# Optimization experiments

Measured on AMD Instinct MI355X. Metric: run time of the kernel, lower is better.

## Reference

```python
import jax, jax.numpy as jnp
import numpy as np

N = 50000      # nodes
E = 600000     # edges
P = 200000     # prediction edges
IN = 128       # in_channels
HID = 128      # hidden per head
H1, H2 = 4, 2  # heads
BN_EPS = 1e-5
NEG_SLOPE = 0.2


def _rn(k, shape, scale=0.05):
    return jax.random.normal(k, shape, jnp.float32) * scale


def setup_inputs() -> dict:
    key = jax.random.key(0)
    ks = jax.random.split(key, 24)
    inp = {}
    inp['x'] = jax.random.normal(ks[0], (N, IN), jnp.float32)
    inp['ei'] = jax.random.randint(ks[1], (2, E), 0, N, dtype=jnp.int32)
    inp['pred_edges'] = jax.random.randint(ks[2], (2, P), 0, N, dtype=jnp.int32)
    inp['pert'] = jax.random.normal(ks[3], (N,), jnp.float32)
    inp['pr'] = jax.random.uniform(ks[4], (N,), jnp.float32)
    # GATv2 layer 1: in=IN -> H1 heads x HID
    inp['Wl1'] = _rn(ks[5], (IN, H1 * HID))
    inp['bl1'] = jnp.zeros((H1 * HID,), jnp.float32)
    inp['Wr1'] = _rn(ks[6], (IN, H1 * HID))
    inp['br1'] = jnp.zeros((H1 * HID,), jnp.float32)
    inp['att1'] = _rn(ks[7], (H1, HID))
    inp['bias1'] = jnp.zeros((H1 * HID,), jnp.float32)
    # BatchNorm1d(H1*HID) eval-mode params
    inp['bn1_g'] = jnp.ones((H1 * HID,), jnp.float32)
    inp['bn1_b'] = jnp.zeros((H1 * HID,), jnp.float32)
    inp['bn1_m'] = _rn(ks[8], (H1 * HID,))
    inp['bn1_v'] = jax.random.uniform(ks[9], (H1 * HID,), jnp.float32, 0.5, 1.5)
    # GATv2 layer 2: in=H1*HID -> H2 heads x HID
    inp['Wl2'] = _rn(ks[10], (H1 * HID, H2 * HID))
    inp['bl2'] = jnp.zeros((H2 * HID,), jnp.float32)
    inp['Wr2'] = _rn(ks[11], (H1 * HID, H2 * HID))
    inp['br2'] = jnp.zeros((H2 * HID,), jnp.float32)
    inp['att2'] = _rn(ks[12], (H2, HID))
    inp['bias2'] = jnp.zeros((H2 * HID,), jnp.float32)
    inp['bn2_g'] = jnp.ones((H2 * HID,), jnp.float32)
    inp['bn2_b'] = jnp.zeros((H2 * HID,), jnp.float32)
    inp['bn2_m'] = _rn(ks[13], (H2 * HID,))
    inp['bn2_v'] = jax.random.uniform(ks[14], (H2 * HID,), jnp.float32, 0.5, 1.5)
    # proj: Linear(H2*HID*2 + 2 + 1, 2)
    inp['Wp'] = _rn(ks[15], (H2 * HID * 2 + 3, 2))
    inp['bp'] = jnp.zeros((2,), jnp.float32)
    return inp


def gatv2(x, src, dst, Wl, bl, Wr, br, att, bias, n):
    """GATv2Conv (concat=True): e_ij = att . LeakyReLU(xl_j + xr_i), segment softmax over dst."""
    H, C = att.shape
    xl = (x @ Wl + bl).reshape(n, H, C)
    xr = (x @ Wr + br).reshape(n, H, C)
    e = jax.nn.leaky_relu(xl[src] + xr[dst], NEG_SLOPE)     # [E, H, C]
    score = jnp.einsum('ehc,hc->eh', e, att)                 # [E, H]
    m = jax.ops.segment_max(score, dst, num_segments=n)     # [N, H]
    ex = jnp.exp(score - m[dst])
    denom = jax.ops.segment_sum(ex, dst, num_segments=n)
    alpha = ex / denom[dst]                                  # [E, H]
    out = jax.ops.segment_sum(alpha[:, :, None] * xl[src], dst, num_segments=n)
    return out.reshape(n, H * C) + bias


def batchnorm_eval(h, g, b, m, v):
    return (h - m) * jax.lax.rsqrt(v + BN_EPS) * g + b


def reference(x, ei, pred_edges, pert, pr,
              Wl1, bl1, Wr1, br1, att1, bias1, bn1_g, bn1_b, bn1_m, bn1_v,
              Wl2, bl2, Wr2, br2, att2, bias2, bn2_g, bn2_b, bn2_m, bn2_v,
              Wp, bp):
    n = x.shape[0]
    loop = jnp.arange(n, dtype=ei.dtype)                    # add_self_loops=True
    src = jnp.concatenate([ei[0], loop])
    dst = jnp.concatenate([ei[1], loop])
    h = gatv2(x, src, dst, Wl1, bl1, Wr1, br1, att1, bias1, n)
    h = jax.nn.relu(batchnorm_eval(h, bn1_g, bn1_b, bn1_m, bn1_v))
    h = gatv2(h, src, dst, Wl2, bl2, Wr2, br2, att2, bias2, n)
    z = jax.nn.relu(batchnorm_eval(h, bn2_g, bn2_b, bn2_m, bn2_v))
    s, d = pred_edges[0], pred_edges[1]
    feat = jnp.concatenate([z[s], z[d], pr[s][:, None], pr[d][:, None],
                            (pert[s] * pert[d])[:, None]], axis=1)
    return feat @ Wp + bp
```

## Files before the change

### kernel.cpp

```cpp
#include <hip/hip_runtime.h>
#include <math.h>

#define BN_EPS 1e-5f
#define N_NODES 50000
#define M_PAD   50048
#define E_EDGES 600000

typedef __attribute__((ext_vector_type(8))) short bf16x8;
typedef __attribute__((ext_vector_type(4))) short bf16x4;
typedef __attribute__((ext_vector_type(4))) float f32x4;

__device__ __forceinline__ short f2bf(float f) {
    unsigned u = __float_as_uint(f);
    u += 0x7fffu + ((u >> 16) & 1u);
    return (short)(u >> 16);
}
__device__ __forceinline__ float bf2f(short s) {
    return __uint_as_float(((unsigned)(unsigned short)s) << 16);
}
__device__ __forceinline__ void gload_lds16(const short* g, short* l) {
    __builtin_amdgcn_global_load_lds((const __attribute__((address_space(1))) void*)g,
                                     (__attribute__((address_space(3))) void*)l, 16, 0, 0);
}

__device__ short g_xlb[(size_t)M_PAD * 512];
__device__ short g_xrb[(size_t)M_PAD * 512];
__device__ short g_h1b[(size_t)M_PAD * 512];
__device__ short g_xb[(size_t)M_PAD * 128];
__device__ short g_zb[(size_t)M_PAD * 256];
__device__ short g_wt[393216];
__device__ int   g_rowptr[N_NODES + 1];
__device__ int   g_bsum[256];
__device__ int   g_cursor[N_NODES];
__device__ int   g_counts[N_NODES];
__device__ int   g_csrc[E_EDGES + N_NODES];


__global__ void k_init_counts(int* __restrict__ counts, int n) {
    int i = blockIdx.x * blockDim.x + threadIdx.x;
    if (i < n) counts[i] = 1;
}

__global__ void k_hist(const int* __restrict__ ei, int E, int* __restrict__ counts) {
    int e = blockIdx.x * blockDim.x + threadIdx.x;
    if (e < E) atomicAdd(&counts[ei[E + e]], 1);
}

__global__ void k_scan1(const int* __restrict__ counts, int n,
                        int* __restrict__ rp, int* __restrict__ bsum) {
    __shared__ int sd[256];
    int t = threadIdx.x;
    int g = blockIdx.x * 256 + t;
    int v = (g < n) ? counts[g] : 0;
    sd[t] = v;
    __syncthreads();
    for (int o = 1; o < 256; o <<= 1) {
        int u = (t >= o) ? sd[t - o] : 0;
        __syncthreads();
        sd[t] += u;
        __syncthreads();
    }
    if (g < n) rp[g + 1] = sd[t];
    if (t == 255) bsum[blockIdx.x] = sd[255];
}

__global__ void k_scan2(int* __restrict__ bsum, int nb) {
    __shared__ int sd[256];
    int t = threadIdx.x;
    int v = (t < nb) ? bsum[t] : 0;
    sd[t] = v;
    __syncthreads();
    for (int o = 1; o < 256; o <<= 1) {
        int u = (t >= o) ? sd[t - o] : 0;
        __syncthreads();
        sd[t] += u;
        __syncthreads();
    }
    if (t < nb) bsum[t] = sd[t] - v;
}

__global__ void k_scan3(int* __restrict__ rp, const int* __restrict__ bsum, int n) {
    int g = blockIdx.x * blockDim.x + threadIdx.x;
    if (g < n) rp[g + 1] += bsum[g >> 8];
    if (g == 0) rp[0] = 0;
}

__global__ void k_fill(const int* __restrict__ rp, int* __restrict__ cursor,
                       int* __restrict__ csrc, int n) {
    int i = blockIdx.x * blockDim.x + threadIdx.x;
    if (i < n) {
        int p = rp[i];
        csrc[p] = i;
        cursor[i] = p + 1;
    }
}

__global__ void k_scatter(const int* __restrict__ ei, int E,
                          int* __restrict__ cursor, int* __restrict__ csrc) {
    int e = blockIdx.x * blockDim.x + threadIdx.x;
    if (e < E) {
        int d = ei[E + e];
        int p = atomicAdd(&cursor[d], 1);
        csrc[p] = ei[e];
    }
}


__global__ void k_f32_to_bf16_v4(const float* __restrict__ in, short* __restrict__ out,
                                 int n4) {
    int i = blockIdx.x * blockDim.x + threadIdx.x;
    if (i < n4) {
        float4 v = ((const float4*)in)[i];
        short4 o;
        o.x = f2bf(v.x); o.y = f2bf(v.y); o.z = f2bf(v.z); o.w = f2bf(v.w);
        ((short4*)out)[i] = o;
    }
}

__global__ void k_transpose_w(const float* __restrict__ W, short* __restrict__ Wt,
                              int K, int N) {
    __shared__ float s[32][33];
    int n0 = blockIdx.x * 32, k0 = blockIdx.y * 32;
    int tx = threadIdx.x, ty = threadIdx.y;
    #pragma unroll
    for (int q = 0; q < 4; q++)
        s[ty * 4 + q][tx] = W[(size_t)(k0 + ty * 4 + q) * N + n0 + tx];
    __syncthreads();
    #pragma unroll
    for (int q = 0; q < 4; q++)
        Wt[(size_t)(n0 + ty * 4 + q) * K + k0 + tx] = f2bf(s[tx][ty * 4 + q]);
}

__global__ __launch_bounds__(256) void k_gemm_dual(
    const short* __restrict__ A, const short* __restrict__ Bt,
    const float* __restrict__ bias_l, const float* __restrict__ bias_r,
    short* __restrict__ Cl, short* __restrict__ Cr,
    int N, int K)
{
    __shared__ short sA[128][64];
    __shared__ short sB0[128][64];
    __shared__ short sB1[128][64];
    int tid = threadIdx.x;
    int wid = tid >> 6, lane = tid & 63;
    int m0 = blockIdx.y * 128;
    int n0 = blockIdx.x * 256;
    int wr = (wid >> 1) * 64;
    int wc = (wid & 1) * 64;
    int rowL = wid * 32 + (lane >> 3);
    int chunk = lane & 7;

    f32x4 acc0[4][4] = {};
    f32x4 acc1[4][4] = {};

    for (int k0 = 0; k0 < K; k0 += 64) {
        #pragma unroll
        for (int i = 0; i < 4; i++) {
            int row = rowL + i * 8;
            int cs = chunk ^ (row & 7);
            const short* ga = A  + ((size_t)(m0 + row) * K + k0 + cs * 8);
            const short* g0 = Bt + ((size_t)(n0 + row) * K + k0 + cs * 8);
            const short* g1 = Bt + ((size_t)(n0 + 128 + row) * K + k0 + cs * 8);
            gload_lds16(ga, &sA[wid * 32 + i * 8][0]);
            gload_lds16(g0, &sB0[wid * 32 + i * 8][0]);
            gload_lds16(g1, &sB1[wid * 32 + i * 8][0]);
        }
        __syncthreads();
        #pragma unroll
        for (int kk = 0; kk < 2; kk++) {
            bf16x8 af[4], bf0[4], bf1[4];
            #pragma unroll
            for (int i = 0; i < 4; i++) {
                int r = wr + i * 16 + (lane & 15);
                int c = ((kk * 4 + (lane >> 4)) ^ (r & 7)) << 3;
                af[i] = *(bf16x8*)&sA[r][c];
            }
            #pragma unroll
            for (int j = 0; j < 4; j++) {
                int r = wc + j * 16 + (lane & 15);
                int c = ((kk * 4 + (lane >> 4)) ^ (r & 7)) << 3;
                bf0[j] = *(bf16x8*)&sB0[r][c];
                bf1[j] = *(bf16x8*)&sB1[r][c];
            }
            #pragma unroll
            for (int i = 0; i < 4; i++)
                #pragma unroll
                for (int j = 0; j < 4; j++) {
                    acc0[i][j] = __builtin_amdgcn_mfma_f32_16x16x32_bf16(
                        bf0[j], af[i], acc0[i][j], 0, 0, 0);
                    acc1[i][j] = __builtin_amdgcn_mfma_f32_16x16x32_bf16(
                        bf1[j], af[i], acc1[i][j], 0, 0, 0);
                }
        }
        __syncthreads();
    }
    short* outp;
    const float* bp2;
    int cb;
    if (n0 < N) { outp = Cl; bp2 = bias_l; cb = n0; }
    else        { outp = Cr; bp2 = bias_r; cb = n0 - N; }
    #pragma unroll
    for (int i = 0; i < 4; i++) {
        int rowg = m0 + wr + i * 16 + (lane & 15);
        #pragma unroll
        for (int j = 0; j < 4; j++) {
            int nl = cb + wc + j * 16 + (lane >> 4) * 4;
            float4 b0 = *(const float4*)(bp2 + nl);
            float4 b1 = *(const float4*)(bp2 + nl + 128);
            short o0[4], o1[4];
            o0[0] = f2bf(acc0[i][j][0] + b0.x); o0[1] = f2bf(acc0[i][j][1] + b0.y);
            o0[2] = f2bf(acc0[i][j][2] + b0.z); o0[3] = f2bf(acc0[i][j][3] + b0.w);
            o1[0] = f2bf(acc1[i][j][0] + b1.x); o1[1] = f2bf(acc1[i][j][1] + b1.y);
            o1[2] = f2bf(acc1[i][j][2] + b1.z); o1[3] = f2bf(acc1[i][j][3] + b1.w);
            *(bf16x4*)(outp + (size_t)rowg * N + nl)       = *(bf16x4*)o0;
            *(bf16x4*)(outp + (size_t)rowg * N + nl + 128) = *(bf16x4*)o1;
        }
    }
}

template <int H, typename OT>
__global__ void k_gat_agg(const short* __restrict__ xl, const short* __restrict__ xr,
                          const float* __restrict__ att,
                          const int* __restrict__ rp, const int* __restrict__ csrc,
                          const float* __restrict__ bias,
                          const float* __restrict__ bng, const float* __restrict__ bnb,
                          const float* __restrict__ bnm, const float* __restrict__ bnv,
                          OT* __restrict__ out, int n) {
    constexpr int G = 64 / H;
    constexpr int CPL = 128 / G;
    const int D = H * 128;
    int wid = (blockIdx.x * blockDim.x + threadIdx.x) >> 6;
    int lane = threadIdx.x & 63;
    if (wid >= n) return;
    const int i = wid;
    const int h = lane / G;
    const int ch0 = h * 128 + (lane % G) * CPL;

    float xrv[CPL], attv[CPL];
    {
        short raw[CPL];
        if constexpr (CPL == 8)
            *(bf16x8*)raw = *(const bf16x8*)(xr + (size_t)i * D + ch0);
        else
            *(bf16x4*)raw = *(const bf16x4*)(xr + (size_t)i * D + ch0);
        #pragma unroll
        for (int q = 0; q < CPL; q++) {
            xrv[q] = bf2f(raw[q]);
            attv[q] = att[ch0 + q];
        }
    }
    float m = -INFINITY, dnm = 0.f, acc[CPL] = {};

    int e0 = rp[i], e1 = rp[i + 1];
    int e = e0;
    for (; e + 3 < e1; e += 4) {
        int j0 = csrc[e], j1 = csrc[e + 1], j2 = csrc[e + 2], j3 = csrc[e + 3];
        float x0[CPL], x1[CPL], x2[CPL], x3[CPL];
        {
            short r0[CPL], r1[CPL], r2[CPL], r3[CPL];
            if constexpr (CPL == 8) {
                *(bf16x8*)r0 = *(const bf16x8*)(xl + (size_t)j0 * D + ch0);
                *(bf16x8*)r1 = *(const bf16x8*)(xl + (size_t)j1 * D + ch0);
                *(bf16x8*)r2 = *(const bf16x8*)(xl + (size_t)j2 * D + ch0);
                *(bf16x8*)r3 = *(const bf16x8*)(xl + (size_t)j3 * D + ch0);
            } else {
                *(bf16x4*)r0 = *(const bf16x4*)(xl + (size_t)j0 * D + ch0);
                *(bf16x4*)r1 = *(const bf16x4*)(xl + (size_t)j1 * D + ch0);
                *(bf16x4*)r2 = *(const bf16x4*)(xl + (size_t)j2 * D + ch0);
                *(bf16x4*)r3 = *(const bf16x4*)(xl + (size_t)j3 * D + ch0);
            }
            #pragma unroll
            for (int q = 0; q < CPL; q++) {
                x0[q] = bf2f(r0[q]); x1[q] = bf2f(r1[q]);
                x2[q] = bf2f(r2[q]); x3[q] = bf2f(r3[q]);
            }
        }
        float p0 = 0.f, p1 = 0.f, p2 = 0.f, p3 = 0.f;
        #pragma unroll
        for (int q = 0; q < CPL; q++) {
            float v0 = x0[q] + xrv[q], v1 = x1[q] + xrv[q];
            float v2 = x2[q] + xrv[q], v3 = x3[q] + xrv[q];
            v0 = fmaxf(v0, 0.2f * v0); v1 = fmaxf(v1, 0.2f * v1);
            v2 = fmaxf(v2, 0.2f * v2); v3 = fmaxf(v3, 0.2f * v3);
            p0 = fmaf(attv[q], v0, p0); p1 = fmaf(attv[q], v1, p1);
            p2 = fmaf(attv[q], v2, p2); p3 = fmaf(attv[q], v3, p3);
        }
        #pragma unroll
        for (int o = G / 2; o > 0; o >>= 1) {
            p0 += __shfl_xor(p0, o, 64);
            p1 += __shfl_xor(p1, o, 64);
            p2 += __shfl_xor(p2, o, 64);
            p3 += __shfl_xor(p3, o, 64);
        }
        float mn = fmaxf(fmaxf(fmaxf(p0, p1), fmaxf(p2, p3)), m);
        float scale = __expf(m - mn);
        float w0 = __expf(p0 - mn), w1 = __expf(p1 - mn);
        float w2 = __expf(p2 - mn), w3 = __expf(p3 - mn);
        dnm = dnm * scale + (w0 + w1) + (w2 + w3);
        #pragma unroll
        for (int q = 0; q < CPL; q++) {
            float a = fmaf(w0, x0[q], acc[q] * scale);
            a = fmaf(w1, x1[q], a);
            a = fmaf(w2, x2[q], a);
            acc[q] = fmaf(w3, x3[q], a);
        }
        m = mn;
    }
    for (; e < e1; e++) {
        int j = csrc[e];
        float xlv[CPL];
        {
            short raw[CPL];
            if constexpr (CPL == 8)
                *(bf16x8*)raw = *(const bf16x8*)(xl + (size_t)j * D + ch0);
            else
                *(bf16x4*)raw = *(const bf16x4*)(xl + (size_t)j * D + ch0);
            #pragma unroll
            for (int q = 0; q < CPL; q++) xlv[q] = bf2f(raw[q]);
        }
        float part = 0.f;
        #pragma unroll
        for (int q = 0; q < CPL; q++) {
            float v = xlv[q] + xrv[q];
            v = fmaxf(v, 0.2f * v);
            part = fmaf(attv[q], v, part);
        }
        #pragma unroll
        for (int o = G / 2; o > 0; o >>= 1) part += __shfl_xor(part, o, 64);
        float mn = fmaxf(m, part);
        float scale = __expf(m - mn);
        float p = __expf(part - mn);
        dnm = dnm * scale + p;
        #pragma unroll
        for (int q = 0; q < CPL; q++) acc[q] = fmaf(p, xlv[q], acc[q] * scale);
        m = mn;
    }

    float inv = 1.f / dnm;
    float res[CPL];
    #pragma unroll
    for (int q = 0; q < CPL; q++) {
        int ch = ch0 + q;
        float o = acc[q] * inv + bias[ch];
        float vv = (o - bnm[ch]) * rsqrtf(bnv[ch] + BN_EPS) * bng[ch] + bnb[ch];
        res[q] = fmaxf(vv, 0.f);
    }
    if constexpr (sizeof(OT) == 2) {
        short ov[CPL];
        #pragma unroll
        for (int q = 0; q < CPL; q++) ov[q] = f2bf(res[q]);
        if constexpr (CPL == 8)
            *(bf16x8*)(out + (size_t)i * D + ch0) = *(bf16x8*)ov;
        else
            *(bf16x4*)(out + (size_t)i * D + ch0) = *(bf16x4*)ov;
    } else {
        #pragma unroll
        for (int q = 0; q < CPL; q++) out[(size_t)i * D + ch0 + q] = res[q];
    }
}

__global__ void k_pred(const short* __restrict__ z, const int* __restrict__ pe,
                       const float* __restrict__ pr, const float* __restrict__ pert,
                       const float* __restrict__ Wp, const float* __restrict__ bp,
                       float* __restrict__ out, int P) {
    int wid = (blockIdx.x * blockDim.x + threadIdx.x) >> 6;
    int lane = threadIdx.x & 63;
    if (wid >= P) return;
    int s = pe[wid], d = pe[P + wid];
    int node = (lane < 32) ? s : d;
    int off = (lane & 31) * 8;
    short raw[8];
    *(bf16x8*)raw = *(const bf16x8*)(z + (size_t)node * 256 + off);
    int fbase = (lane < 32) ? off : 256 + off;
    float a0 = 0.f, a1 = 0.f;
    #pragma unroll
    for (int q = 0; q < 8; q++) {
        float v = bf2f(raw[q]);
        a0 = fmaf(v, Wp[(fbase + q) * 2 + 0], a0);
        a1 = fmaf(v, Wp[(fbase + q) * 2 + 1], a1);
    }
    #pragma unroll
    for (int o = 32; o > 0; o >>= 1) {
        a0 += __shfl_xor(a0, o, 64);
        a1 += __shfl_xor(a1, o, 64);
    }
    if (lane == 0) {
        float prs = pr[s], prd = pr[d], pp = pert[s] * pert[d];
        a0 += prs * Wp[512 * 2 + 0] + prd * Wp[513 * 2 + 0] + pp * Wp[514 * 2 + 0] + bp[0];
        a1 += prs * Wp[512 * 2 + 1] + prd * Wp[513 * 2 + 1] + pp * Wp[514 * 2 + 1] + bp[1];
        *(float2*)(out + (size_t)wid * 2) = make_float2(a0, a1);
    }
}


extern "C" void kernel_launch(void* const* d_in, const int* in_sizes, int n_in,
                              void* d_out, int out_size, void* d_ws, size_t ws_size,
                              hipStream_t stream) {
    const float* x    = (const float*)d_in[0];
    const int*   ei   = (const int*)d_in[1];
    const int*   pe   = (const int*)d_in[2];
    const float* pert = (const float*)d_in[3];
    const float* pr   = (const float*)d_in[4];
    const float* Wl1  = (const float*)d_in[5];
    const float* bl1  = (const float*)d_in[6];
    const float* Wr1  = (const float*)d_in[7];
    const float* br1  = (const float*)d_in[8];
    const float* att1 = (const float*)d_in[9];
    const float* bias1= (const float*)d_in[10];
    const float* bn1g = (const float*)d_in[11];
    const float* bn1b = (const float*)d_in[12];
    const float* bn1m = (const float*)d_in[13];
    const float* bn1v = (const float*)d_in[14];
    const float* Wl2  = (const float*)d_in[15];
    const float* bl2  = (const float*)d_in[16];
    const float* Wr2  = (const float*)d_in[17];
    const float* br2  = (const float*)d_in[18];
    const float* att2 = (const float*)d_in[19];
    const float* bias2= (const float*)d_in[20];
    const float* bn2g = (const float*)d_in[21];
    const float* bn2b = (const float*)d_in[22];
    const float* bn2m = (const float*)d_in[23];
    const float* bn2v = (const float*)d_in[24];
    const float* Wp   = (const float*)d_in[25];
    const float* bp   = (const float*)d_in[26];

    const int n  = in_sizes[3];
    const int E  = in_sizes[1] / 2;
    const int P  = in_sizes[2] / 2;
    const int IN = in_sizes[0] / n;
    const int D1 = 512, D2 = 256;

    static short* xlb = nullptr;
    static short* xrb = nullptr;
    static short* h1b = nullptr;
    static short* xb  = nullptr;
    static short* zb  = nullptr;
    static short* wt  = nullptr;
    static int *rowptr = nullptr, *bsum = nullptr, *cursor = nullptr,
               *counts = nullptr, *csrc = nullptr;
    if (!xlb) {
        hipGetSymbolAddress((void**)&xlb,    HIP_SYMBOL(g_xlb));
        hipGetSymbolAddress((void**)&xrb,    HIP_SYMBOL(g_xrb));
        hipGetSymbolAddress((void**)&h1b,    HIP_SYMBOL(g_h1b));
        hipGetSymbolAddress((void**)&xb,     HIP_SYMBOL(g_xb));
        hipGetSymbolAddress((void**)&zb,     HIP_SYMBOL(g_zb));
        hipGetSymbolAddress((void**)&wt,     HIP_SYMBOL(g_wt));
        hipGetSymbolAddress((void**)&rowptr, HIP_SYMBOL(g_rowptr));
        hipGetSymbolAddress((void**)&bsum,   HIP_SYMBOL(g_bsum));
        hipGetSymbolAddress((void**)&cursor, HIP_SYMBOL(g_cursor));
        hipGetSymbolAddress((void**)&counts, HIP_SYMBOL(g_counts));
        hipGetSymbolAddress((void**)&csrc,   HIP_SYMBOL(g_csrc));
    }

    short* xl1b = xlb;
    short* xr1b = xrb;
    short* xl2b = xlb;
    short* xr2b = xlb + (size_t)M_PAD * D2;
    short* WtL1 = wt;
    short* WtL2 = wt + 131072;
    short* Wl1t = wt;
    short* Wr1t = wt + 65536;
    short* Wl2t = wt + 131072;
    short* Wr2t = wt + 262144;

    const int nb = (n + 255) / 256;

    k_init_counts<<<nb, 256, 0, stream>>>(counts, n);
    k_hist<<<(E + 255) / 256, 256, 0, stream>>>(ei, E, counts);
    k_scan1<<<nb, 256, 0, stream>>>(counts, n, rowptr, bsum);
    k_scan2<<<1, 256, 0, stream>>>(bsum, nb);
    k_scan3<<<nb, 256, 0, stream>>>(rowptr, bsum, n);
    k_fill<<<nb, 256, 0, stream>>>(rowptr, cursor, csrc, n);
    k_scatter<<<(E + 255) / 256, 256, 0, stream>>>(ei, E, cursor, csrc);

    {
        int n4 = n * IN / 4;
        k_f32_to_bf16_v4<<<(n4 + 255) / 256, 256, 0, stream>>>(x, xb, n4);
        k_transpose_w<<<dim3(D1 / 32, IN / 32), dim3(32, 8), 0, stream>>>(Wl1, Wl1t, IN, D1);
        k_transpose_w<<<dim3(D1 / 32, IN / 32), dim3(32, 8), 0, stream>>>(Wr1, Wr1t, IN, D1);
        k_transpose_w<<<dim3(D2 / 32, D1 / 32), dim3(32, 8), 0, stream>>>(Wl2, Wl2t, D1, D2);
        k_transpose_w<<<dim3(D2 / 32, D1 / 32), dim3(32, 8), 0, stream>>>(Wr2, Wr2t, D1, D2);
    }

    const int mb = M_PAD / 128;

    k_gemm_dual<<<dim3(2 * D1 / 256, mb), 256, 0, stream>>>(
        xb, WtL1, bl1, br1, xl1b, xr1b, D1, IN);
    k_gat_agg<4, short><<<(n + 3) / 4, 256, 0, stream>>>(xl1b, xr1b, att1, rowptr, csrc,
                                                  bias1, bn1g, bn1b, bn1m, bn1v, h1b, n);
    k_gemm_dual<<<dim3(2 * D2 / 256, mb), 256, 0, stream>>>(
        h1b, WtL2, bl2, br2, xl2b, xr2b, D2, D1);
    k_gat_agg<2, short><<<(n + 3) / 4, 256, 0, stream>>>(xl2b, xr2b, att2, rowptr, csrc,
                                                  bias2, bn2g, bn2b, bn2m, bn2v, zb, n);
    k_pred<<<(P + 3) / 4, 256, 0, stream>>>(zb, pe, pr, pert, Wp, bp,
                                            (float*)d_out, P);
}
```

Before: 617.5 us.

## Precompute per-node projection of z before edge prediction; unroll aggregation by two

Because the final linear layer distributes over the concatenation, the prediction stage now projects each node's z vector once, onto the source and destination halves of Wp, into a small per-node buffer. A per-edge kernel then only gathers two float4 values instead of reading two 256-wide rows for each of 200k prediction edges. The GAT aggregation loop also drops from 4-edge to 2-edge unrolling, which lowers register pressure but leaves fewer loads in flight. This adds one kernel launch and a 50k x 4 float buffer.

Result: faster. 572.2 us (-7.3%).

```diff
diff --git a/kernel.cpp b/kernel.cpp
--- a/kernel.cpp
+++ b/kernel.cpp
@@ -28,6 +28,7 @@
 __device__ short g_h1b[(size_t)M_PAD * 512];
 __device__ short g_xb[(size_t)M_PAD * 128];
 __device__ short g_zb[(size_t)M_PAD * 256];
+__device__ float g_y[(size_t)M_PAD * 4];
 __device__ short g_wt[393216];
 __device__ int   g_rowptr[N_NODES + 1];
 __device__ int   g_bsum[256];
@@ -252,60 +253,47 @@
 
     int e0 = rp[i], e1 = rp[i + 1];
     int e = e0;
-    for (; e + 3 < e1; e += 4) {
-        int j0 = csrc[e], j1 = csrc[e + 1], j2 = csrc[e + 2], j3 = csrc[e + 3];
-        float x0[CPL], x1[CPL], x2[CPL], x3[CPL];
+    for (; e + 1 < e1; e += 2) {
+        int j0 = csrc[e], j1 = csrc[e + 1];
+        float xlv0[CPL], xlv1[CPL];
         {
-            short r0[CPL], r1[CPL], r2[CPL], r3[CPL];
+            short r0[CPL], r1[CPL];
             if constexpr (CPL == 8) {
                 *(bf16x8*)r0 = *(const bf16x8*)(xl + (size_t)j0 * D + ch0);
                 *(bf16x8*)r1 = *(const bf16x8*)(xl + (size_t)j1 * D + ch0);
-                *(bf16x8*)r2 = *(const bf16x8*)(xl + (size_t)j2 * D + ch0);
-                *(bf16x8*)r3 = *(const bf16x8*)(xl + (size_t)j3 * D + ch0);
             } else {
                 *(bf16x4*)r0 = *(const bf16x4*)(xl + (size_t)j0 * D + ch0);
                 *(bf16x4*)r1 = *(const bf16x4*)(xl + (size_t)j1 * D + ch0);
-                *(bf16x4*)r2 = *(const bf16x4*)(xl + (size_t)j2 * D + ch0);
-                *(bf16x4*)r3 = *(const bf16x4*)(xl + (size_t)j3 * D + ch0);
             }
             #pragma unroll
-            for (int q = 0; q < CPL; q++) {
-                x0[q] = bf2f(r0[q]); x1[q] = bf2f(r1[q]);
-                x2[q] = bf2f(r2[q]); x3[q] = bf2f(r3[q]);
-            }
-        }
-        float p0 = 0.f, p1 = 0.f, p2 = 0.f, p3 = 0.f;
+            for (int q = 0; q < CPL; q++) { xlv0[q] = bf2f(r0[q]); xlv1[q] = bf2f(r1[q]); }
+        }
+        float p0 = 0.f, p1 = 0.f;
         #pragma unroll
         for (int q = 0; q < CPL; q++) {
-            float v0 = x0[q] + xrv[q], v1 = x1[q] + xrv[q];
-            float v2 = x2[q] + xrv[q], v3 = x3[q] + xrv[q];
-            v0 = fmaxf(v0, 0.2f * v0); v1 = fmaxf(v1, 0.2f * v1);
-            v2 = fmaxf(v2, 0.2f * v2); v3 = fmaxf(v3, 0.2f * v3);
-            p0 = fmaf(attv[q], v0, p0); p1 = fmaf(attv[q], v1, p1);
-            p2 = fmaf(attv[q], v2, p2); p3 = fmaf(attv[q], v3, p3);
+            float v0 = xlv0[q] + xrv[q];
+            float v1 = xlv1[q] + xrv[q];
+            v0 = fmaxf(v0, 0.2f * v0);
+            v1 = fmaxf(v1, 0.2f * v1);
+            p0 = fmaf(attv[q], v0, p0);
+            p1 = fmaf(attv[q], v1, p1);
         }
         #pragma unroll
         for (int o = G / 2; o > 0; o >>= 1) {
             p0 += __shfl_xor(p0, o, 64);
             p1 += __shfl_xor(p1, o, 64);
-            p2 += __shfl_xor(p2, o, 64);
-            p3 += __shfl_xor(p3, o, 64);
-        }
-        float mn = fmaxf(fmaxf(fmaxf(p0, p1), fmaxf(p2, p3)), m);
+        }
+        float mn = fmaxf(m, fmaxf(p0, p1));
         float scale = __expf(m - mn);
-        float w0 = __expf(p0 - mn), w1 = __expf(p1 - mn);
-        float w2 = __expf(p2 - mn), w3 = __expf(p3 - mn);
-        dnm = dnm * scale + (w0 + w1) + (w2 + w3);
-        #pragma unroll
-        for (int q = 0; q < CPL; q++) {
-            float a = fmaf(w0, x0[q], acc[q] * scale);
-            a = fmaf(w1, x1[q], a);
-            a = fmaf(w2, x2[q], a);
-            acc[q] = fmaf(w3, x3[q], a);
-        }
+        float w0 = __expf(p0 - mn);
+        float w1 = __expf(p1 - mn);
+        dnm = dnm * scale + w0 + w1;
+        #pragma unroll
+        for (int q = 0; q < CPL; q++)
+            acc[q] = fmaf(w1, xlv1[q], fmaf(w0, xlv0[q], acc[q] * scale));
         m = mn;
     }
-    for (; e < e1; e++) {
+    if (e < e1) {
         int j = csrc[e];
         float xlv[CPL];
         {
@@ -358,37 +346,47 @@
     }
 }
 
-__global__ void k_pred(const short* __restrict__ z, const int* __restrict__ pe,
-                       const float* __restrict__ pr, const float* __restrict__ pert,
-                       const float* __restrict__ Wp, const float* __restrict__ bp,
-                       float* __restrict__ out, int P) {
+__global__ void k_zproj(const short* __restrict__ z, const float* __restrict__ Wp,
+                        float* __restrict__ y, int n) {
     int wid = (blockIdx.x * blockDim.x + threadIdx.x) >> 6;
     int lane = threadIdx.x & 63;
-    if (wid >= P) return;
-    int s = pe[wid], d = pe[P + wid];
-    int node = (lane < 32) ? s : d;
-    int off = (lane & 31) * 8;
-    short raw[8];
-    *(bf16x8*)raw = *(const bf16x8*)(z + (size_t)node * 256 + off);
-    int fbase = (lane < 32) ? off : 256 + off;
-    float a0 = 0.f, a1 = 0.f;
-    #pragma unroll
-    for (int q = 0; q < 8; q++) {
+    if (wid >= n) return;
+    int ch = lane * 4;
+    short raw[4];
+    *(bf16x4*)raw = *(const bf16x4*)(z + (size_t)wid * 256 + ch);
+    float a0 = 0.f, a1 = 0.f, a2 = 0.f, a3 = 0.f;
+    #pragma unroll
+    for (int q = 0; q < 4; q++) {
         float v = bf2f(raw[q]);
-        a0 = fmaf(v, Wp[(fbase + q) * 2 + 0], a0);
-        a1 = fmaf(v, Wp[(fbase + q) * 2 + 1], a1);
+        a0 = fmaf(v, Wp[(ch + q) * 2 + 0], a0);
+        a1 = fmaf(v, Wp[(ch + q) * 2 + 1], a1);
+        a2 = fmaf(v, Wp[(256 + ch + q) * 2 + 0], a2);
+        a3 = fmaf(v, Wp[(256 + ch + q) * 2 + 1], a3);
     }
     #pragma unroll
     for (int o = 32; o > 0; o >>= 1) {
         a0 += __shfl_xor(a0, o, 64);
         a1 += __shfl_xor(a1, o, 64);
-    }
-    if (lane == 0) {
-        float prs = pr[s], prd = pr[d], pp = pert[s] * pert[d];
-        a0 += prs * Wp[512 * 2 + 0] + prd * Wp[513 * 2 + 0] + pp * Wp[514 * 2 + 0] + bp[0];
-        a1 += prs * Wp[512 * 2 + 1] + prd * Wp[513 * 2 + 1] + pp * Wp[514 * 2 + 1] + bp[1];
-        *(float2*)(out + (size_t)wid * 2) = make_float2(a0, a1);
-    }
+        a2 += __shfl_xor(a2, o, 64);
+        a3 += __shfl_xor(a3, o, 64);
+    }
+    if (lane == 0)
+        *(float4*)(y + (size_t)wid * 4) = make_float4(a0, a1, a2, a3);
+}
+
+__global__ void k_pred_edge(const float* __restrict__ y, const int* __restrict__ pe,
+                            const float* __restrict__ pr, const float* __restrict__ pert,
+                            const float* __restrict__ Wp, const float* __restrict__ bp,
+                            float* __restrict__ out, int P) {
+    int e = blockIdx.x * blockDim.x + threadIdx.x;
+    if (e >= P) return;
+    int s = pe[e], d = pe[P + e];
+    float4 ys = *(const float4*)(y + (size_t)s * 4);
+    float4 yd = *(const float4*)(y + (size_t)d * 4);
+    float prs = pr[s], prd = pr[d], pp = pert[s] * pert[d];
+    float o0 = ys.x + yd.z + prs * Wp[1024] + prd * Wp[1026] + pp * Wp[1028] + bp[0];
+    float o1 = ys.y + yd.w + prs * Wp[1025] + prd * Wp[1027] + pp * Wp[1029] + bp[1];
+    *(float2*)(out + (size_t)e * 2) = make_float2(o0, o1);
 }
 
 
@@ -434,6 +432,7 @@
     static short* h1b = nullptr;
     static short* xb  = nullptr;
     static short* zb  = nullptr;
+    static float* yv  = nullptr;
     static short* wt  = nullptr;
     static int *rowptr = nullptr, *bsum = nullptr, *cursor = nullptr,
                *counts = nullptr, *csrc = nullptr;
@@ -443,6 +442,7 @@
         hipGetSymbolAddress((void**)&h1b,    HIP_SYMBOL(g_h1b));
         hipGetSymbolAddress((void**)&xb,     HIP_SYMBOL(g_xb));
         hipGetSymbolAddress((void**)&zb,     HIP_SYMBOL(g_zb));
+        hipGetSymbolAddress((void**)&yv,     HIP_SYMBOL(g_y));
         hipGetSymbolAddress((void**)&wt,     HIP_SYMBOL(g_wt));
         hipGetSymbolAddress((void**)&rowptr, HIP_SYMBOL(g_rowptr));
         hipGetSymbolAddress((void**)&bsum,   HIP_SYMBOL(g_bsum));
@@ -491,6 +491,7 @@
         h1b, WtL2, bl2, br2, xl2b, xr2b, D2, D1);
     k_gat_agg<2, short><<<(n + 3) / 4, 256, 0, stream>>>(xl2b, xr2b, att2, rowptr, csrc,
                                                   bias2, bn2g, bn2b, bn2m, bn2v, zb, n);
-    k_pred<<<(P + 3) / 4, 256, 0, stream>>>(zb, pe, pr, pert, Wp, bp,
-                                            (float*)d_out, P);
-}
+    k_zproj<<<(n + 3) / 4, 256, 0, stream>>>(zb, Wp, yv, n);
+    k_pred_edge<<<(P + 255) / 256, 256, 0, stream>>>(yv, pe, pr, pert, Wp, bp,
+                                                     (float*)d_out, P);
+}
```
